# Kernel tuning notes

Hardware: AMD Instinct MI355X
Metric: run time of the kernel (lower is better)

Reference implementation:

```python
import jax, jax.numpy as jnp
import numpy as np

N, M, S = 1536, 1536, 3
POS = ((-1, -1), (-1, 0), (0, -1))  # match, X (gap in y), Y (gap in x)
NEG_INF = -1.0e8  # matches the torch implementation's neg_inf literal


def _hmm_forward(theta):
    """Smoothed-max (softmax operator) forward DP over a 3-state pair HMM.

    theta: (N, M, S, S) combined transition+emission potentials.
    V[i, j, s] = logsumexp_k( V[i+di_s, j+dj_s, k] + theta[i-1, j-1, s, k] )
    Vt = logsumexp_k V[N, M, k]
    Implemented as a row scan (dependence on previous row) with an inner
    column scan (dependence on V[i, j-1] via the Y state).
    """
    n, m, s, _ = theta.shape
    # V[0, :] border: V[0,0] = 0 (all states), rest -inf
    init_row = jnp.full((m + 1, s), NEG_INF, theta.dtype).at[0].set(0.0)
    v_border = jnp.full((s,), NEG_INF, theta.dtype)  # V[i, 0]

    def col_step(v_left, inputs):
        diag, up, th = inputs  # V[i-1,j-1](S,), V[i-1,j](S,), theta[i-1,j-1](S,S)
        # row s of src = predecessor V-vector selected by pos[s]
        src = jnp.stack([diag if p == (-1, -1) else (up if p == (-1, 0) else v_left)
                         for p in POS])          # (S, S)
        v_new = jax.nn.logsumexp(src + th, axis=-1)  # (S,)
        return v_new, v_new

    def row_step(prev_row, theta_row):
        # prev_row: (M+1, S) = V[i-1, :]; theta_row: (M, S, S)
        _, vals = jax.lax.scan(col_step, v_border,
                               (prev_row[:-1], prev_row[1:], theta_row))
        new_row = jnp.concatenate([v_border[None], vals], axis=0)  # (M+1, S)
        return new_row, None

    last_row, _ = jax.lax.scan(row_step, init_row, theta)
    # terminal smoothed max over V[N, M]
    return jax.nn.logsumexp(last_row[m])


def setup_inputs() -> dict:
    key = jax.random.key(0)
    theta = jax.random.normal(key, (N, M, S, S), dtype=jnp.float32)
    return {"theta": theta}


def reference(theta):
    return _hmm_forward(theta)
```

## Files before the change

### kernel.cpp

```cpp
#include <hip/hip_runtime.h>


#define MM 1536
#define HH 64
#define NB 24
#define U  8
#define NBLK 200
#define NSTEP 1608
#define LOG2E 1.4426950408889634f
#define LN2   0.6931471805599453f
#define NEG2  (-1.4426950408889634e8f)

#define LDS_TH  4608
#define LDS_FD  9216
#define LDS_FDB 64

typedef float f32x4 __attribute__((ext_vector_type(4)));
typedef float f32x2 __attribute__((ext_vector_type(2)));

template <int BYTES>
__device__ __forceinline__ void gl_lds(const float* g, float* l) {
    auto* gp = (const __attribute__((address_space(1))) float*)(g);
    auto* lp = (__attribute__((address_space(3))) float*)(l);
    if constexpr (BYTES == 16) __builtin_amdgcn_global_load_lds(gp, lp, 16, 0, 0);
    else                       __builtin_amdgcn_global_load_lds(gp, lp, 4, 0, 0);
}

__device__ __forceinline__ float shup1(float x) {
    int xi = __builtin_bit_cast(int, x);
    int r  = __builtin_amdgcn_update_dpp(xi, xi, 0x138, 0xF, 0xF, false);
    return __builtin_bit_cast(float, r);
}

__device__ __forceinline__ float lse3_2(float a, float b, float c) {
    float mx = fmaxf(fmaxf(a, b), c);
    float mn = fminf(fminf(a, b), c);
    float md = __builtin_amdgcn_fmed3f(a, b, c);
    return mx + __builtin_amdgcn_logf(1.0f + __builtin_amdgcn_exp2f(mn - mx)
                                           + __builtin_amdgcn_exp2f(md - mx));
}

__global__ void init_progress_kernel(int* progress) {
    if (threadIdx.x < NB) progress[threadIdx.x] = -1;
}

__global__ __launch_bounds__(256)
void skew_kernel(const float* __restrict__ theta, float* __restrict__ skew)
{
    const int wid  = blockIdx.x * 4 + (threadIdx.x >> 6);
    const int lane = threadIdx.x & 63;
    const int b = wid / NSTEP;
    const int t = wid - b * NSTEP;

    const int c = t - lane;
    float v[9];
    if ((unsigned)c < (unsigned)MM) {
        const float* g = theta + ((size_t)(b * HH + lane) * MM + c) * 9;
        __builtin_memcpy(&v[0], g, 36);
    } else {
        #pragma unroll
        for (int i = 0; i < 9; ++i) v[i] = 0.0f;
    }

    float* o = skew + (size_t)(b * NSTEP + t) * 576;
    f32x4 a; a.x = v[0]; a.y = v[1]; a.z = v[2]; a.w = v[3];
    f32x4 q; q.x = v[4]; q.y = v[5]; q.z = v[6]; q.w = v[7];
    *(f32x4*)(o + lane * 4)       = a;
    *(f32x4*)(o + 256 + lane * 4) = q;
    o[512 + lane] = v[8];
}

template <bool SKEW>
__global__ __launch_bounds__(64, 1)
void hmm_fwd_kernel(const float* __restrict__ src, float* __restrict__ out,
                    float* __restrict__ bottom, int* __restrict__ progress)
{
    __shared__ __align__(16) float smem[2 * LDS_TH + 2 * LDS_FDB];

    const int b    = blockIdx.x;
    const int lane = threadIdx.x;
    const float* __restrict__ thp =
        SKEW ? nullptr : src + (size_t)(b * HH + lane) * (MM * 9);
    const float* __restrict__ skp =
        SKEW ? src + (size_t)b * NSTEP * 576 : nullptr;
    const float* __restrict__ bsrc =
        bottom + (size_t)(b > 0 ? b - 1 : 0) * ((MM + 1) * 3);
    float* __restrict__ bdst = bottom + (size_t)b * ((MM + 1) * 3);

    float d0, d1, d2, l0, l1, l2, s0, s1, s2, res0, res1, res2;
    d0 = d1 = d2 = (b == 0 && lane == 0) ? 0.0f : NEG2;
    l0 = l1 = l2 = NEG2;
    s0 = s1 = s2 = NEG2;
    res0 = res1 = res2 = NEG2;

    const int fidx = lane < 24 ? lane : 23;
    const int fk   = fidx / 3;
    const int fr   = fidx - fk * 3;

    auto issue_block = [&](int tb, int nbuf) {
        if constexpr (SKEW) {
            const float* g0 = skp + (size_t)tb * 576 + lane * 4;
            float* l0_ = &smem[nbuf * LDS_TH];
            #pragma unroll
            for (int d = 0; d < 18; ++d)
                gl_lds<16>(g0 + d * 256, l0_ + d * 256);
        } else {
            #pragma unroll
            for (int k = 0; k < U; ++k) {
                int c = tb + k - lane;
                c = c < 0 ? 0 : (c > MM - 1 ? MM - 1 : c);
                const float* g = thp + (size_t)c * 9;
                float* base = &smem[nbuf * LDS_TH + k * 576];
                gl_lds<16>(g,     base);
                gl_lds<16>(g + 4, base + 256);
                gl_lds<4 >(g + 8, base + 512);
            }
        }
        if (b > 0) {
            int jn = tb + fk + 1; if (jn > MM) jn = MM;
            gl_lds<4>(bsrc + (size_t)jn * 3 + fr, &smem[LDS_FD + nbuf * LDS_FDB]);
        }
    };

    if (b > 0) {
        while (__hip_atomic_load(&progress[b - 1], __ATOMIC_ACQUIRE,
                                 __HIP_MEMORY_SCOPE_AGENT) < 24)
            __builtin_amdgcn_s_sleep(2);
    }

    issue_block(0, 0);
    asm volatile("s_waitcnt vmcnt(0)" ::: "memory");
    __builtin_amdgcn_sched_barrier(0);

    auto block_body = [&](int T, int cb, bool mlo, bool mhi) {
        const int t0 = T * U;
        const int nbuf = cb ^ 1;

        if (b > 0 && T > 0 && (T & 1) == 0) {
            int need = t0 + 24; if (need > MM) need = MM;
            while (__hip_atomic_load(&progress[b - 1], __ATOMIC_ACQUIRE,
                                     __HIP_MEMORY_SCOPE_AGENT) < need)
                __builtin_amdgcn_s_sleep(2);
        }

        if (b < NB - 1) asm volatile("s_waitcnt vmcnt(16)" ::: "memory");
        else            asm volatile("s_waitcnt vmcnt(0)"  ::: "memory");

        issue_block(t0 + U, nbuf);

        if (b < NB - 1 && lane == HH - 1) {
            int val = t0 - 71;
            if (val >= 1) {
                if (val > MM) val = MM;
                __hip_atomic_store(&progress[b], val, __ATOMIC_RELAXED,
                                   __HIP_MEMORY_SCOPE_AGENT);
            }
        }
        __builtin_amdgcn_sched_barrier(0);

        const float* base  = &smem[cb * LDS_TH];
        const float* fbase = &smem[LDS_FD + cb * LDS_FDB];
        f32x4 q0 = *(const f32x4*)(base + lane * 4);
        f32x4 q1 = *(const f32x4*)(base + 256 + lane * 4);
        float s8 = base[512 + lane];
        float f0 = NEG2, f1 = NEG2, f2 = NEG2;
        if (b > 0) { f0 = fbase[0]; f1 = fbase[1]; f2 = fbase[2]; }

        #pragma unroll
        for (int k = 0; k < U; ++k) {
            f32x4 q0n, q1n; float s8n, f0n = NEG2, f1n = NEG2, f2n = NEG2;
            if (k < U - 1) {
                const float* cp = base + (k + 1) * 576;
                q0n = *(const f32x4*)(cp + lane * 4);
                q1n = *(const f32x4*)(cp + 256 + lane * 4);
                s8n = cp[512 + lane];
                if (b > 0) {
                    f0n = fbase[(k + 1) * 3];
                    f1n = fbase[(k + 1) * 3 + 1];
                    f2n = fbase[(k + 1) * 3 + 2];
                }
            }

            const int c = t0 + k - lane;
            bool act = true;
            if (mlo || mhi) act = ((unsigned)c < (unsigned)MM);

            float u0 = (lane == 0) ? f0 : s0;
            float u1 = (lane == 0) ? f1 : s1;
            float u2 = (lane == 0) ? f2 : s2;

            float aa0 = fmaf(q0.x, LOG2E, d0);
            float aa1 = fmaf(q0.y, LOG2E, d1);
            float aa2 = fmaf(q0.z, LOG2E, d2);
            float bb0 = fmaf(q0.w, LOG2E, u0);
            float bb1 = fmaf(q1.x, LOG2E, u1);
            float bb2 = fmaf(q1.y, LOG2E, u2);
            float cc0 = fmaf(q1.z, LOG2E, l0);
            float cc1 = fmaf(q1.w, LOG2E, l1);
            float cc2 = fmaf(s8,   LOG2E, l2);

            float n0 = lse3_2(aa0, aa1, aa2);
            float n1 = lse3_2(bb0, bb1, bb2);
            float n2 = lse3_2(cc0, cc1, cc2);
            if (mlo || mhi) {
                n0 = act ? n0 : NEG2;
                n1 = act ? n1 : NEG2;
                n2 = act ? n2 : NEG2;
            }

            if (b < NB - 1 && lane == HH - 1) {
                int j = c + 1;
                if (mlo || mhi) j = act ? c + 1 : 0;
                float* sa = bdst + (size_t)j * 3;
                f32x2 p01; p01.x = n0; p01.y = n1;
                asm volatile("global_store_dwordx2 %0, %1, off sc1"
                             :: "v"(sa), "v"(p01) : "memory");
                asm volatile("global_store_dword %0, %1, off offset:8 sc1"
                             :: "v"(sa), "v"(n2) : "memory");
            }

            if (mhi) {
                const bool fin = (c == MM - 1);
                res0 = fin ? n0 : res0;
                res1 = fin ? n1 : res1;
                res2 = fin ? n2 : res2;
            }

            d0 = u0; d1 = u1; d2 = u2;
            s0 = shup1(n0);
            s1 = shup1(n1);
            s2 = shup1(n2);
            l0 = n0; l1 = n1; l2 = n2;

            if (k < U - 1) {
                q0 = q0n; q1 = q1n; s8 = s8n;
                f0 = f0n; f1 = f1n; f2 = f2n;
            }
        }
    };

    for (int T = 0;   T < 8;    ++T) block_body(T, T & 1, true,  false);
    for (int T = 8;   T < 192;  ++T) block_body(T, T & 1, false, false);
    for (int T = 192; T < NBLK; ++T) block_body(T, T & 1, false, true);

    if (b < NB - 1 && lane == HH - 1) {
        asm volatile("s_waitcnt vmcnt(0)" ::: "memory");
        __hip_atomic_store(&progress[b], MM, __ATOMIC_RELEASE,
                           __HIP_MEMORY_SCOPE_AGENT);
    }

    if (b == NB - 1 && lane == HH - 1)
        out[0] = LN2 * lse3_2(res0, res1, res2);
}

extern "C" void kernel_launch(void* const* d_in, const int* in_sizes, int n_in,
                              void* d_out, int out_size, void* d_ws, size_t ws_size,
                              hipStream_t stream)
{
    const float* theta = (const float*)d_in[0];
    float* out = (float*)d_out;

    const size_t skew_fl = (size_t)NB * NSTEP * 576;
    const size_t bot_fl  = (size_t)NB * (MM + 1) * 3;
    const size_t need    = (skew_fl + bot_fl) * sizeof(float) + NB * sizeof(int);

    if (ws_size >= need) {
        float* skew     = (float*)d_ws;
        float* bottom   = skew + skew_fl;
        int*   progress = (int*)(bottom + bot_fl);
        init_progress_kernel<<<1, 64, 0, stream>>>(progress);
        skew_kernel<<<(NB * NSTEP) / 4, 256, 0, stream>>>(theta, skew);
        hmm_fwd_kernel<true><<<NB, HH, 0, stream>>>(skew, out, bottom, progress);
    } else {
        float* bottom   = (float*)d_ws;
        int*   progress = (int*)((char*)d_ws + bot_fl * sizeof(float));
        init_progress_kernel<<<1, 64, 0, stream>>>(progress);
        hmm_fwd_kernel<false><<<NB, HH, 0, stream>>>(theta, out, bottom, progress);
    }
}
```

Baseline: 1.040 ms.

## Prefetch theta and boundary feeds directly into double-buffered registers instead of LDS

Drops the LDS staging, which used global_load_lds into two shared-memory buffers. Each wave now loads its theta records and the upper block's boundary values straight into two register arrays. The block loop is unrolled by two so the arrays swap roles without copies. The aim is to take the per-step LDS reads off the serial recurrence. The cost is much higher VGPR usage. Because the inline-asm loads are invisible to the compiler's wait-count tracking, the hand-written vmcnt(16) waits may no longer be enough to guarantee the data has arrived.

```diff
diff --git a/kernel.cpp b/kernel.cpp
--- a/kernel.cpp
+++ b/kernel.cpp
@@ -11,20 +11,11 @@
 #define LN2   0.6931471805599453f
 #define NEG2  (-1.4426950408889634e8f)
 
-#define LDS_TH  4608
-#define LDS_FD  9216
-#define LDS_FDB 64
-
 typedef float f32x4 __attribute__((ext_vector_type(4)));
 typedef float f32x2 __attribute__((ext_vector_type(2)));
 
-template <int BYTES>
-__device__ __forceinline__ void gl_lds(const float* g, float* l) {
-    auto* gp = (const __attribute__((address_space(1))) float*)(g);
-    auto* lp = (__attribute__((address_space(3))) float*)(l);
-    if constexpr (BYTES == 16) __builtin_amdgcn_global_load_lds(gp, lp, 16, 0, 0);
-    else                       __builtin_amdgcn_global_load_lds(gp, lp, 4, 0, 0);
-}
+struct T9R { f32x4 q0; f32x4 q1; float s8; };
+struct F3R { float v0, v1, v2; };
 
 __device__ __forceinline__ float shup1(float x) {
     int xi = __builtin_bit_cast(int, x);
@@ -75,8 +66,6 @@
 void hmm_fwd_kernel(const float* __restrict__ src, float* __restrict__ out,
                     float* __restrict__ bottom, int* __restrict__ progress)
 {
-    __shared__ __align__(16) float smem[2 * LDS_TH + 2 * LDS_FDB];
-
     const int b    = blockIdx.x;
     const int lane = threadIdx.x;
     const float* __restrict__ thp =
@@ -93,32 +82,51 @@
     s0 = s1 = s2 = NEG2;
     res0 = res1 = res2 = NEG2;
 
-    const int fidx = lane < 24 ? lane : 23;
-    const int fk   = fidx / 3;
-    const int fr   = fidx - fk * 3;
-
-    auto issue_block = [&](int tb, int nbuf) {
+    T9R thA[U], thB[U];
+    F3R fdA[U], fdB[U];
+    #pragma unroll
+    for (int k = 0; k < U; ++k) {
+        fdA[k].v0 = fdA[k].v1 = fdA[k].v2 = NEG2;
+        fdB[k].v0 = fdB[k].v1 = fdB[k].v2 = NEG2;
+    }
+
+    auto issue_theta = [&](int tb, T9R (&nx)[U]) {
         if constexpr (SKEW) {
-            const float* g0 = skp + (size_t)tb * 576 + lane * 4;
-            float* l0_ = &smem[nbuf * LDS_TH];
             #pragma unroll
-            for (int d = 0; d < 18; ++d)
-                gl_lds<16>(g0 + d * 256, l0_ + d * 256);
+            for (int k = 0; k < U; ++k) {
+                const float* rec = skp + (size_t)(tb + k) * 576;
+                const float* aq  = rec + (size_t)lane * 4;
+                const float* as_ = rec + 512 + lane;
+                asm volatile("global_load_dwordx4 %0, %1, off"
+                             : "=v"(nx[k].q0) : "v"(aq));
+                asm volatile("global_load_dwordx4 %0, %1, off offset:1024"
+                             : "=v"(nx[k].q1) : "v"(aq));
+                asm volatile("global_load_dword %0, %1, off"
+                             : "=v"(nx[k].s8) : "v"(as_));
+            }
         } else {
             #pragma unroll
             for (int k = 0; k < U; ++k) {
                 int c = tb + k - lane;
                 c = c < 0 ? 0 : (c > MM - 1 ? MM - 1 : c);
-                const float* g = thp + (size_t)c * 9;
-                float* base = &smem[nbuf * LDS_TH + k * 576];
-                gl_lds<16>(g,     base);
-                gl_lds<16>(g + 4, base + 256);
-                gl_lds<4 >(g + 8, base + 512);
-            }
-        }
+                __builtin_memcpy(&thA[0], &thA[0], 0);
+                struct P { float f[9]; } tmp;
+                __builtin_memcpy(&tmp, thp + (size_t)c * 9, 36);
+                nx[k].q0.x = tmp.f[0]; nx[k].q0.y = tmp.f[1];
+                nx[k].q0.z = tmp.f[2]; nx[k].q0.w = tmp.f[3];
+                nx[k].q1.x = tmp.f[4]; nx[k].q1.y = tmp.f[5];
+                nx[k].q1.z = tmp.f[6]; nx[k].q1.w = tmp.f[7];
+                nx[k].s8   = tmp.f[8];
+            }
+        }
+    };
+    auto issue_feed = [&](int tb, F3R (&fx)[U]) {
         if (b > 0) {
-            int jn = tb + fk + 1; if (jn > MM) jn = MM;
-            gl_lds<4>(bsrc + (size_t)jn * 3 + fr, &smem[LDS_FD + nbuf * LDS_FDB]);
+            #pragma unroll
+            for (int k = 0; k < U; ++k) {
+                int jn = tb + k + 1; if (jn > MM) jn = MM;
+                __builtin_memcpy(&fx[k], bsrc + (size_t)jn * 3, 12);
+            }
         }
     };
 
@@ -128,13 +136,15 @@
             __builtin_amdgcn_s_sleep(2);
     }
 
-    issue_block(0, 0);
+    issue_theta(0, thA);
+    issue_feed(0, fdA);
     asm volatile("s_waitcnt vmcnt(0)" ::: "memory");
     __builtin_amdgcn_sched_barrier(0);
 
-    auto block_body = [&](int T, int cb, bool mlo, bool mhi) {
+    auto block_body = [&](int T, T9R (&cur)[U], T9R (&nxt)[U],
+                          F3R (&fcur)[U], F3R (&fnxt)[U],
+                          bool mlo, bool mhi) {
         const int t0 = T * U;
-        const int nbuf = cb ^ 1;
 
         if (b > 0 && T > 0 && (T & 1) == 0) {
             int need = t0 + 24; if (need > MM) need = MM;
@@ -146,7 +156,8 @@
         if (b < NB - 1) asm volatile("s_waitcnt vmcnt(16)" ::: "memory");
         else            asm volatile("s_waitcnt vmcnt(0)"  ::: "memory");
 
-        issue_block(t0 + U, nbuf);
+        issue_theta(t0 + U, nxt);
+        issue_feed(t0 + U, fnxt);
 
         if (b < NB - 1 && lane == HH - 1) {
             int val = t0 - 71;
@@ -158,46 +169,25 @@
         }
         __builtin_amdgcn_sched_barrier(0);
 
-        const float* base  = &smem[cb * LDS_TH];
-        const float* fbase = &smem[LDS_FD + cb * LDS_FDB];
-        f32x4 q0 = *(const f32x4*)(base + lane * 4);
-        f32x4 q1 = *(const f32x4*)(base + 256 + lane * 4);
-        float s8 = base[512 + lane];
-        float f0 = NEG2, f1 = NEG2, f2 = NEG2;
-        if (b > 0) { f0 = fbase[0]; f1 = fbase[1]; f2 = fbase[2]; }
-
         #pragma unroll
         for (int k = 0; k < U; ++k) {
-            f32x4 q0n, q1n; float s8n, f0n = NEG2, f1n = NEG2, f2n = NEG2;
-            if (k < U - 1) {
-                const float* cp = base + (k + 1) * 576;
-                q0n = *(const f32x4*)(cp + lane * 4);
-                q1n = *(const f32x4*)(cp + 256 + lane * 4);
-                s8n = cp[512 + lane];
-                if (b > 0) {
-                    f0n = fbase[(k + 1) * 3];
-                    f1n = fbase[(k + 1) * 3 + 1];
-                    f2n = fbase[(k + 1) * 3 + 2];
-                }
-            }
-
             const int c = t0 + k - lane;
             bool act = true;
             if (mlo || mhi) act = ((unsigned)c < (unsigned)MM);
 
-            float u0 = (lane == 0) ? f0 : s0;
-            float u1 = (lane == 0) ? f1 : s1;
-            float u2 = (lane == 0) ? f2 : s2;
-
-            float aa0 = fmaf(q0.x, LOG2E, d0);
-            float aa1 = fmaf(q0.y, LOG2E, d1);
-            float aa2 = fmaf(q0.z, LOG2E, d2);
-            float bb0 = fmaf(q0.w, LOG2E, u0);
-            float bb1 = fmaf(q1.x, LOG2E, u1);
-            float bb2 = fmaf(q1.y, LOG2E, u2);
-            float cc0 = fmaf(q1.z, LOG2E, l0);
-            float cc1 = fmaf(q1.w, LOG2E, l1);
-            float cc2 = fmaf(s8,   LOG2E, l2);
+            float u0 = (lane == 0) ? fcur[k].v0 : s0;
+            float u1 = (lane == 0) ? fcur[k].v1 : s1;
+            float u2 = (lane == 0) ? fcur[k].v2 : s2;
+
+            float aa0 = fmaf(cur[k].q0.x, LOG2E, d0);
+            float aa1 = fmaf(cur[k].q0.y, LOG2E, d1);
+            float aa2 = fmaf(cur[k].q0.z, LOG2E, d2);
+            float bb0 = fmaf(cur[k].q0.w, LOG2E, u0);
+            float bb1 = fmaf(cur[k].q1.x, LOG2E, u1);
+            float bb2 = fmaf(cur[k].q1.y, LOG2E, u2);
+            float cc0 = fmaf(cur[k].q1.z, LOG2E, l0);
+            float cc1 = fmaf(cur[k].q1.w, LOG2E, l1);
+            float cc2 = fmaf(cur[k].s8,   LOG2E, l2);
 
             float n0 = lse3_2(aa0, aa1, aa2);
             float n1 = lse3_2(bb0, bb1, bb2);
@@ -231,17 +221,21 @@
             s1 = shup1(n1);
             s2 = shup1(n2);
             l0 = n0; l1 = n1; l2 = n2;
-
-            if (k < U - 1) {
-                q0 = q0n; q1 = q1n; s8 = s8n;
-                f0 = f0n; f1 = f1n; f2 = f2n;
-            }
         }
     };
 
-    for (int T = 0;   T < 8;    ++T) block_body(T, T & 1, true,  false);
-    for (int T = 8;   T < 192;  ++T) block_body(T, T & 1, false, false);
-    for (int T = 192; T < NBLK; ++T) block_body(T, T & 1, false, true);
+    for (int T = 0; T < 8; T += 2) {
+        block_body(T,     thA, thB, fdA, fdB, true, false);
+        block_body(T + 1, thB, thA, fdB, fdA, true, false);
+    }
+    for (int T = 8; T < 192; T += 2) {
+        block_body(T,     thA, thB, fdA, fdB, false, false);
+        block_body(T + 1, thB, thA, fdB, fdA, false, false);
+    }
+    for (int T = 192; T < NBLK; T += 2) {
+        block_body(T,     thA, thB, fdA, fdB, false, true);
+        block_body(T + 1, thB, thA, fdB, fdA, false, true);
+    }
 
     if (b < NB - 1 && lane == HH - 1) {
         asm volatile("s_waitcnt vmcnt(0)" ::: "memory");
```

Result: faster. 1.005 ms (-3.4%).
